# Performance work log

Hardware: AMD Instinct MI355X
Metric: run time of the kernel (lower is better)

## Reference

```python
import jax, jax.numpy as jnp
import numpy as np

B, D, E = 4096, 768, 8
L = (32 // E) * D  # per-expert latents = 3072
K = 32             # topk


def setup_inputs() -> dict:
    key = jax.random.key(0)
    ks = jax.random.split(key, 8)
    x = jax.random.normal(ks[0], (B, D), dtype=jnp.float32)
    router_w = jax.random.normal(ks[1], (E, D), dtype=jnp.float32) / np.sqrt(D)
    router_b = jnp.zeros((E,), dtype=jnp.float32)
    W_enc = jax.random.normal(ks[2], (E, L, D), dtype=jnp.float32) / np.sqrt(D)
    b_enc = jnp.zeros((E, L), dtype=jnp.float32)
    W_dec = jax.random.normal(ks[3], (E, L, D), dtype=jnp.float32)
    # normalize_decoder=True: unit-norm decoder rows
    W_dec = W_dec / jnp.linalg.norm(W_dec, axis=-1, keepdims=True)
    b_dec = jnp.zeros((E, D), dtype=jnp.float32)
    return {"x": x, "router_w": router_w, "router_b": router_b,
            "W_enc": W_enc, "b_enc": b_enc, "W_dec": W_dec, "b_dec": b_dec}


def reference(x, router_w, router_b, W_enc, b_enc, W_dec, b_dec):
    Bx = x.shape[0]
    # --- router (top-1) ---
    logits = x @ router_w.T + router_b            # [B, E]
    expert_ids = jnp.argmax(logits, axis=-1)      # [B]
    probs = jax.nn.softmax(logits, axis=-1)
    sel_probs = jnp.max(probs, axis=-1)           # prob of argmax expert

    # --- load-balance loss ---
    counts = jnp.zeros((E,), jnp.float32).at[expert_ids].add(1.0)
    freq = counts / Bx
    load_balance_loss = jnp.sum((freq - 1.0 / E) ** 2)

    sae_out = jnp.zeros_like(x)
    latent_acts = jnp.zeros((Bx, K), x.dtype)
    latent_indices = jnp.zeros((Bx, K), jnp.int32)
    total_fvu = jnp.float32(0.0)
    rows = jnp.arange(Bx)[:, None]

    for e in range(E):  # fixed small expert loop
        mask = expert_ids == e                    # [B]
        mf = mask.astype(x.dtype)[:, None]        # [B,1]
        n = jnp.sum(mf)
        # encode: TopK SAE, pre-acts on (x - b_dec)
        pre = jax.nn.relu((x - b_dec[e]) @ W_enc[e].T + b_enc[e])   # [B, L]
        acts, idx = jax.lax.top_k(pre, K)                            # [B, K]
        # decode via dense sparse-latent matmul
        z = jnp.zeros((Bx, L), x.dtype).at[rows, idx].set(acts)      # [B, L]
        recon = z @ W_dec[e] + b_dec[e]                              # [B, D]
        # combine: weight by router prob, scatter by mask
        sae_out = sae_out + mf * recon * sel_probs[:, None]
        latent_acts = jnp.where(mask[:, None], acts, latent_acts)
        latent_indices = jnp.where(mask[:, None], idx, latent_indices)
        # per-expert FVU over its tokens (unweighted reconstruction)
        mean_e = jnp.sum(x * mf, axis=0) / jnp.maximum(n, 1.0)
        var_e = jnp.sum(mf * (x - mean_e) ** 2)
        l2_e = jnp.sum(mf * (x - recon) ** 2)
        fvu_e = jnp.where((n > 0) & (var_e > 0), l2_e / jnp.maximum(var_e, 1e-12), 0.0)
        total_fvu = total_fvu + fvu_e * n

    fvu = total_fvu / Bx
    auxk_loss = jnp.float32(0.0)       # dead_mask=None
    multi_topk_fvu = jnp.float32(0.0)  # multi_topk=False
    return (sae_out, latent_acts, latent_indices, fvu, auxk_loss,
            multi_topk_fvu, expert_ids, load_balance_loss)
```

## Files before the change

kernel.cpp:

```cpp
#include <hip/hip_runtime.h>
#include <math.h>

#define B_TOK 4096
#define D_DIM 768
#define E_NUM 8
#define L_LAT 3072
#define K_TOP 32

#define O_SAE  0
#define O_ACTS (B_TOK*D_DIM)
#define O_IDX  (O_ACTS + B_TOK*K_TOP)
#define O_FVU  (O_IDX + B_TOK*K_TOP)
#define O_AUX  (O_FVU + 1)
#define O_MTK  (O_AUX + 1)
#define O_EID  (O_MTK + 1)
#define O_LBL  (O_EID + B_TOK)

struct Ws {
  double S[E_NUM][D_DIM];
  double S2[E_NUM][D_DIM];
  double var_[E_NUM];
  double l2[E_NUM];
  float  sel[B_TOK];
  int    eid[B_TOK];
  int    perm[B_TOK];
  int    counts[E_NUM];
  int    off[E_NUM + 1];
  int    ytab_e[48];
  int    ytab_y[48];
  int    nslots;
  int    pad[15];
};

__global__ void init_k(Ws* ws, float* out) {
  int tid = threadIdx.x;
  if (tid < E_NUM) { ws->counts[tid] = 0; ws->l2[tid] = 0.0; }
  if (tid == 0) { out[O_AUX] = 0.0f; out[O_MTK] = 0.0f; }
}

__global__ void router_k(const float* __restrict__ x, const float* __restrict__ rw,
                         const float* __restrict__ rb, Ws* ws, float* out) {
  int t = blockIdx.x;
  int lane = threadIdx.x;
  double acc[E_NUM];
#pragma unroll
  for (int e = 0; e < E_NUM; ++e) acc[e] = 0.0;
  const float* xr = x + (size_t)t * D_DIM;
#pragma unroll
  for (int j = 0; j < D_DIM / 64; ++j) {
    int d = lane + 64 * j;
    float xv = xr[d];
#pragma unroll
    for (int e = 0; e < E_NUM; ++e) acc[e] += (double)xv * (double)rw[e * D_DIM + d];
  }
#pragma unroll
  for (int e = 0; e < E_NUM; ++e) {
#pragma unroll
    for (int o = 32; o; o >>= 1) acc[e] += __shfl_down(acc[e], o);
  }
  if (lane == 0) {
    double lg[E_NUM];
    int be = 0; double bm = -1e300;
#pragma unroll
    for (int e = 0; e < E_NUM; ++e) {
      lg[e] = acc[e] + (double)rb[e];
      if (lg[e] > bm) { bm = lg[e]; be = e; }
    }
    double s = 0.0;
#pragma unroll
    for (int e = 0; e < E_NUM; ++e) s += exp(lg[e] - bm);
    ws->sel[t] = (float)(1.0 / s);
    ws->eid[t] = be;
    atomicAdd(&ws->counts[be], 1);
    out[O_EID + t] = (float)be;
  }
}

__global__ void scan_k(Ws* ws, float* out) {
  if (threadIdx.x == 0) {
    int o = 0; double loss = 0.0;
    int slot = 0;
    for (int e = 0; e < E_NUM; ++e) {
      ws->off[e] = o;
      int c = ws->counts[e];
      o += c;
      double f = (double)c / (double)B_TOK - 1.0 / (double)E_NUM;
      loss += f * f;
      int nb = (c + 127) / 128;
      for (int b = 0; b < nb; ++b) { ws->ytab_e[slot] = e; ws->ytab_y[slot] = b; ++slot; }
    }
    ws->off[E_NUM] = o;
    ws->nslots = slot;
    out[O_LBL] = (float)loss;
  }
}

__global__ void group_k(Ws* ws) {
  int e = blockIdx.x, tid = threadIdx.x;
  __shared__ int cnt[256];
  const int CH = B_TOK / 256;
  int i0 = tid * CH;
  int c = 0;
#pragma unroll
  for (int i = 0; i < CH; ++i) c += (ws->eid[i0 + i] == e) ? 1 : 0;
  cnt[tid] = c;
  __syncthreads();
  int excl = 0;
  for (int i = 0; i < tid; ++i) excl += cnt[i];
  int base = ws->off[e] + excl;
  for (int i = 0; i < CH; ++i) {
    int t = i0 + i;
    if (ws->eid[t] == e) ws->perm[base++] = t;
  }
}

__global__ void stats_k(const float* __restrict__ x, Ws* ws) {
  int e = blockIdx.x, dg = blockIdx.y;
  int tid = threadIdx.x;
  int dl = tid & 31, strip = tid >> 5;
  int d = dg * 32 + dl;
  int s0 = ws->off[e], s1 = ws->off[e + 1];
  double S = 0.0, S2 = 0.0;
  for (int i = s0 + strip; i < s1; i += 8) {
    float xv = x[(size_t)ws->perm[i] * D_DIM + d];
    S += (double)xv;
    S2 += (double)xv * (double)xv;
  }
  __shared__ double sS[256], sS2[256];
  sS[tid] = S; sS2[tid] = S2;
  __syncthreads();
  for (int s = 128; s >= 32; s >>= 1) {
    if (tid < s) { sS[tid] += sS[tid + s]; sS2[tid] += sS2[tid + s]; }
    __syncthreads();
  }
  if (tid < 32) { ws->S[e][d] = sS[tid]; ws->S2[e][d] = sS2[tid]; }
}

__global__ void var_k(Ws* ws) {
  int e = blockIdx.x, tid = threadIdx.x;
  int n = ws->counts[e];
  double nd = (double)((n > 0) ? n : 1);
  double acc = 0.0;
  for (int d = tid; d < D_DIM; d += 256) {
    double S = ws->S[e][d], S2 = ws->S2[e][d];
    double m = S / nd;
    acc += S2 - 2.0 * m * S + (double)n * m * m;
  }
  __shared__ double red[256];
  red[tid] = acc;
  __syncthreads();
  for (int s = 128; s; s >>= 1) {
    if (tid < s) red[tid] += red[tid + s];
    __syncthreads();
  }
  if (tid == 0) ws->var_[e] = red[0];
}

#define KTILE(ACC, K0) do {                                                    \
  __syncthreads();                                                             \
  _Pragma("unroll")                                                            \
  for (int p = 0; p < 4; ++p) {                                                \
    int idx = p * 256 + tid;                                                   \
    int r = idx >> 3, c4 = (idx & 7) * 4;                                      \
    float4 xv = *(const float4*)(x + (size_t)tokrow[r] * D_DIM + (K0) + c4);   \
    float4 bv = *(const float4*)(bdec + e * D_DIM + (K0) + c4);                \
    float4 xm = make_float4(xv.x - bv.x, xv.y - bv.y, xv.z - bv.z, xv.w - bv.w);\
    *(float4*)&xs[r][c4] = xm;                                                 \
    *(float4*)&wsh[r][c4] =                                                    \
        *(const float4*)(We + wb + (size_t)(bl + r) * D_DIM + (K0) + c4);      \
  }                                                                            \
  __syncthreads();                                                             \
  _Pragma("unroll")                                                            \
  for (int q = 0; q < 8; ++q) {                                                \
    float4 a[8], b[8];                                                         \
    _Pragma("unroll")                                                          \
    for (int i = 0; i < 8; ++i) a[i] = *(const float4*)&xs[ty + 16 * i][q * 4];\
    _Pragma("unroll")                                                          \
    for (int j = 0; j < 8; ++j) b[j] = *(const float4*)&wsh[tx + 16 * j][q * 4];\
    _Pragma("unroll")                                                          \
    for (int i = 0; i < 8; ++i) {                                              \
      _Pragma("unroll")                                                        \
      for (int j = 0; j < 8; ++j) {                                            \
        ACC[i][j] = fmaf(a[i].x, b[j].x, ACC[i][j]);                           \
        ACC[i][j] = fmaf(a[i].y, b[j].y, ACC[i][j]);                           \
        ACC[i][j] = fmaf(a[i].z, b[j].z, ACC[i][j]);                           \
        ACC[i][j] = fmaf(a[i].w, b[j].w, ACC[i][j]);                           \
      }                                                                        \
    }                                                                          \
  }                                                                            \
} while (0)

__launch_bounds__(256, 2)
__global__ void gemm_k(const float* __restrict__ x, const float* __restrict__ We,
                       const float* __restrict__ benc, const float* __restrict__ bdec,
                       Ws* ws, float* __restrict__ pre) {
  int slot = blockIdx.y;
  if (slot >= ws->nslots) return;
  int e = ws->ytab_e[slot];
  int bt = ws->ytab_y[slot] * 128;
  int n0 = ws->off[e], n1 = ws->off[e + 1];
  int ne = n1 - n0;
  int bl = blockIdx.x * 128;

  __shared__ float xs[128][36];
  __shared__ float wsh[128][36];
  __shared__ int tokrow[128];

  int tid = threadIdx.x;
  if (tid < 128) {
    int srow = bt + tid;
    tokrow[tid] = ws->perm[n0 + (srow < ne ? srow : 0)];
  }

  int tx = tid & 15, ty = tid >> 4;
  size_t wb = (size_t)e * L_LAT * D_DIM;

  float acc1[8][8] = {{0.f}}, acc2[8][8] = {{0.f}};

  for (int k0 = 0;   k0 < 512; k0 += 32) KTILE(acc1, k0);
  for (int k0 = 512; k0 < 768; k0 += 32) KTILE(acc2, k0);

#pragma unroll
  for (int i = 0; i < 8; ++i) {
    int srow = bt + ty + 16 * i;
    if (srow < ne) {
      float* pr = &pre[(size_t)(n0 + srow) * L_LAT + bl];
#pragma unroll
      for (int j = 0; j < 8; ++j) {
        int lc = tx + 16 * j;
        float r = (acc1[i][j] + acc2[i][j]) + benc[e * L_LAT + bl + lc];
        pr[lc] = fmaxf(r, 0.0f);
      }
    }
  }
}

__launch_bounds__(256)
__global__ void topk_k(const float* __restrict__ pre, Ws* ws, float* out) {
  __shared__ float buf[4][L_LAT];
  int tid = threadIdx.x, wave = tid >> 6, lane = tid & 63;
  int s = blockIdx.x * 4 + wave;
  int t = ws->perm[s];
  const float* src = pre + (size_t)s * L_LAT;

  unsigned long long bk = 0ULL;
#pragma unroll
  for (int j = 0; j < L_LAT / 256; ++j) {
    int l = lane * 4 + 256 * j;
    float4 v = *(const float4*)(src + l);
    *(float4*)&buf[wave][l] = v;
    const float* vp = &v.x;
#pragma unroll
    for (int c = 0; c < 4; ++c) {
      unsigned long long key = ((unsigned long long)__float_as_uint(vp[c]) << 32)
                             | (unsigned long long)(0xFFFFFFFFu - (unsigned)(l + c));
      if (key > bk) bk = key;
    }
  }

  for (int k = 0; k < K_TOP; ++k) {
    unsigned long long m = bk;
#pragma unroll
    for (int o = 32; o; o >>= 1) {
      unsigned long long o2 = __shfl_down(m, o);
      if (o2 > m) m = o2;
    }
    m = __shfl(m, 0);
    int l = (int)(0xFFFFFFFFu - (unsigned)(m & 0xFFFFFFFFull));
    float v = __uint_as_float((unsigned)(m >> 32));
    if (lane == 0) {
      out[O_ACTS + (size_t)t * K_TOP + k] = v;
      out[O_IDX + (size_t)t * K_TOP + k] = (float)l;
    }
    if (((l >> 2) & 63) == lane) {
      buf[wave][l] = -1.0f;
      bk = 0ULL;
#pragma unroll
      for (int j = 0; j < L_LAT / 256; ++j) {
        int ll = lane * 4 + 256 * j;
        float4 vv = *(const float4*)&buf[wave][ll];
        const float* vp = &vv.x;
#pragma unroll
        for (int c = 0; c < 4; ++c) {
          if (vp[c] >= 0.0f) {
            unsigned long long key = ((unsigned long long)__float_as_uint(vp[c]) << 32)
                                   | (unsigned long long)(0xFFFFFFFFu - (unsigned)(ll + c));
            if (key > bk) bk = key;
          }
        }
      }
    }
  }
}

__launch_bounds__(192)
__global__ void decode_k(const float* __restrict__ x, const float* __restrict__ Wdec,
                         const float* __restrict__ bdec, Ws* ws, float* out) {
  int t = blockIdx.x, tid = threadIdx.x;
  int e = ws->eid[t];
  float sp = ws->sel[t];
  __shared__ float sa[K_TOP];
  __shared__ int si[K_TOP];
  if (tid < K_TOP) {
    sa[tid] = out[O_ACTS + (size_t)t * K_TOP + tid];
    si[tid] = (int)out[O_IDX + (size_t)t * K_TOP + tid];
  }
  __syncthreads();
  int d4 = tid * 4;
  float4 r = make_float4(0.f, 0.f, 0.f, 0.f);
  const float* wdb = Wdec + (size_t)e * L_LAT * D_DIM;
#pragma unroll 8
  for (int k = 0; k < K_TOP; ++k) {
    float4 w = *(const float4*)(wdb + (size_t)si[k] * D_DIM + d4);
    float a = sa[k];
    r.x = fmaf(a, w.x, r.x);
    r.y = fmaf(a, w.y, r.y);
    r.z = fmaf(a, w.z, r.z);
    r.w = fmaf(a, w.w, r.w);
  }
  float4 bd = *(const float4*)(bdec + e * D_DIM + d4);
  float4 rec = make_float4(r.x + bd.x, r.y + bd.y, r.z + bd.z, r.w + bd.w);
  float4 xr = *(const float4*)(x + (size_t)t * D_DIM + d4);
  float4 so = make_float4(rec.x * sp, rec.y * sp, rec.z * sp, rec.w * sp);
  *(float4*)&out[O_SAE + (size_t)t * D_DIM + d4] = so;
  double d0 = (double)(xr.x - rec.x);
  double d1 = (double)(xr.y - rec.y);
  double d2 = (double)(xr.z - rec.z);
  double d3 = (double)(xr.w - rec.w);
  double l2p = d0 * d0 + d1 * d1 + d2 * d2 + d3 * d3;
  __shared__ double red[192];
  red[tid] = l2p;
  __syncthreads();
  for (int s = 96; s >= 3; s >>= 1) {
    if (tid < s) red[tid] += red[tid + s];
    __syncthreads();
  }
  if (tid == 0) atomicAdd(&ws->l2[e], red[0] + red[1] + red[2]);
}

__global__ void final_k(Ws* ws, float* out) {
  if (threadIdx.x == 0) {
    double tot = 0.0;
    for (int e = 0; e < E_NUM; ++e) {
      int n = ws->counts[e];
      double v = ws->var_[e];
      if (n > 0 && v > 0.0) tot += ws->l2[e] / fmax(v, 1e-12) * (double)n;
    }
    out[O_FVU] = (float)(tot / (double)B_TOK);
  }
}

extern "C" void kernel_launch(void* const* d_in, const int* in_sizes, int n_in,
                              void* d_out, int out_size, void* d_ws, size_t ws_size,
                              hipStream_t stream) {
  const float* x  = (const float*)d_in[0];
  const float* rw = (const float*)d_in[1];
  const float* rb = (const float*)d_in[2];
  const float* We = (const float*)d_in[3];
  const float* be = (const float*)d_in[4];
  const float* Wd = (const float*)d_in[5];
  const float* bd = (const float*)d_in[6];
  float* out = (float*)d_out;
  Ws* ws = (Ws*)d_ws;
  float* pre = (float*)((char*)d_ws + ((sizeof(Ws) + 255) & ~(size_t)255));

  hipLaunchKernelGGL(init_k,   dim3(1),           dim3(64),  0, stream, ws, out);
  hipLaunchKernelGGL(router_k, dim3(B_TOK),       dim3(64),  0, stream, x, rw, rb, ws, out);
  hipLaunchKernelGGL(scan_k,   dim3(1),           dim3(64),  0, stream, ws, out);
  hipLaunchKernelGGL(group_k,  dim3(E_NUM),       dim3(256), 0, stream, ws);
  hipLaunchKernelGGL(stats_k,  dim3(E_NUM, 24),   dim3(256), 0, stream, x, ws);
  hipLaunchKernelGGL(gemm_k,   dim3(24, 40),      dim3(256), 0, stream, x, We, be, bd, ws, pre);
  hipLaunchKernelGGL(var_k,    dim3(E_NUM),       dim3(256), 0, stream, ws);
  hipLaunchKernelGGL(topk_k,   dim3(B_TOK / 4),   dim3(256), 0, stream, pre, ws, out);
  hipLaunchKernelGGL(decode_k, dim3(B_TOK),       dim3(192), 0, stream, x, Wd, bd, ws, out);
  hipLaunchKernelGGL(final_k,  dim3(1),           dim3(64),  0, stream, ws, out);
}
```

Baseline: 706.3 us.

## Cut GEMM register pressure and process decode tokens in expert-sorted order

The GEMM inner loop now loads one B operand at a time instead of holding eight, and keeps a single accumulator tile instead of two. The partial sum over the first 512 K columns is written to global memory and read back for the final bias-plus-ReLU. Together these lower register use so the kernel can reach its launch-bound occupancy without spilling, at the cost of an extra global store and load of the pre-activation tile. Separately, the decode kernel walks tokens in the expert-sorted permutation order so neighbouring blocks read the same expert's decoder weights, which should improve cache locality.

```diff
diff --git a/kernel.cpp b/kernel.cpp
--- a/kernel.cpp
+++ b/kernel.cpp
@@ -172,19 +172,18 @@
   __syncthreads();                                                             \
   _Pragma("unroll")                                                            \
   for (int q = 0; q < 8; ++q) {                                                \
-    float4 a[8], b[8];                                                         \
+    float4 a[8];                                                               \
     _Pragma("unroll")                                                          \
     for (int i = 0; i < 8; ++i) a[i] = *(const float4*)&xs[ty + 16 * i][q * 4];\
     _Pragma("unroll")                                                          \
-    for (int j = 0; j < 8; ++j) b[j] = *(const float4*)&wsh[tx + 16 * j][q * 4];\
-    _Pragma("unroll")                                                          \
-    for (int i = 0; i < 8; ++i) {                                              \
+    for (int j = 0; j < 8; ++j) {                                              \
+      float4 b = *(const float4*)&wsh[tx + 16 * j][q * 4];                     \
       _Pragma("unroll")                                                        \
-      for (int j = 0; j < 8; ++j) {                                            \
-        ACC[i][j] = fmaf(a[i].x, b[j].x, ACC[i][j]);                           \
-        ACC[i][j] = fmaf(a[i].y, b[j].y, ACC[i][j]);                           \
-        ACC[i][j] = fmaf(a[i].z, b[j].z, ACC[i][j]);                           \
-        ACC[i][j] = fmaf(a[i].w, b[j].w, ACC[i][j]);                           \
+      for (int i = 0; i < 8; ++i) {                                            \
+        ACC[i][j] = fmaf(a[i].x, b.x, ACC[i][j]);                              \
+        ACC[i][j] = fmaf(a[i].y, b.y, ACC[i][j]);                              \
+        ACC[i][j] = fmaf(a[i].z, b.z, ACC[i][j]);                              \
+        ACC[i][j] = fmaf(a[i].w, b.w, ACC[i][j]);                              \
       }                                                                        \
     }                                                                          \
   }                                                                            \
@@ -215,20 +214,34 @@
   int tx = tid & 15, ty = tid >> 4;
   size_t wb = (size_t)e * L_LAT * D_DIM;
 
-  float acc1[8][8] = {{0.f}}, acc2[8][8] = {{0.f}};
-
-  for (int k0 = 0;   k0 < 512; k0 += 32) KTILE(acc1, k0);
-  for (int k0 = 512; k0 < 768; k0 += 32) KTILE(acc2, k0);
-
+  float acc[8][8] = {{0.f}};
+
+  for (int k0 = 0; k0 < 512; k0 += 32) KTILE(acc, k0);
 #pragma unroll
   for (int i = 0; i < 8; ++i) {
     int srow = bt + ty + 16 * i;
     if (srow < ne) {
       float* pr = &pre[(size_t)(n0 + srow) * L_LAT + bl];
 #pragma unroll
+      for (int j = 0; j < 8; ++j) pr[tx + 16 * j] = acc[i][j];
+    }
+  }
+
+#pragma unroll
+  for (int i = 0; i < 8; ++i)
+#pragma unroll
+    for (int j = 0; j < 8; ++j) acc[i][j] = 0.f;
+  for (int k0 = 512; k0 < 768; k0 += 32) KTILE(acc, k0);
+
+#pragma unroll
+  for (int i = 0; i < 8; ++i) {
+    int srow = bt + ty + 16 * i;
+    if (srow < ne) {
+      float* pr = &pre[(size_t)(n0 + srow) * L_LAT + bl];
+#pragma unroll
       for (int j = 0; j < 8; ++j) {
         int lc = tx + 16 * j;
-        float r = (acc1[i][j] + acc2[i][j]) + benc[e * L_LAT + bl + lc];
+        float r = (pr[lc] + acc[i][j]) + benc[e * L_LAT + bl + lc];
         pr[lc] = fmaxf(r, 0.0f);
       }
     }
@@ -296,7 +309,8 @@
 __launch_bounds__(192)
 __global__ void decode_k(const float* __restrict__ x, const float* __restrict__ Wdec,
                          const float* __restrict__ bdec, Ws* ws, float* out) {
-  int t = blockIdx.x, tid = threadIdx.x;
+  int s = blockIdx.x, tid = threadIdx.x;
+  int t = ws->perm[s];
   int e = ws->eid[t];
   float sp = ws->sel[t];
   __shared__ float sa[K_TOP];
@@ -331,8 +345,8 @@
   __shared__ double red[192];
   red[tid] = l2p;
   __syncthreads();
-  for (int s = 96; s >= 3; s >>= 1) {
-    if (tid < s) red[tid] += red[tid + s];
+  for (int s2 = 96; s2 >= 3; s2 >>= 1) {
+    if (tid < s2) red[tid] += red[tid + s2];
     __syncthreads();
   }
   if (tid == 0) atomicAdd(&ws->l2[e], red[0] + red[1] + red[2]);
```

New measurement: 703.9 us. Within noise of the previous version (-0.3%).
